# Optimization experiments

Measured on AMD Instinct MI355X. Metric: run time of the kernel, lower is better.

## Reference

```python
import jax, jax.numpy as jnp
import numpy as np

B, LQ, LK, D = 8, 2048, 2048, 512
NEG = -1e9  # stands in for -inf; avoids nan in grads, same softmax result


def setup_inputs() -> dict:
    key = jax.random.key(0)
    kq, kk, kv, km, kr = jax.random.split(key, 5)
    q = jax.random.normal(kq, (B, LQ, D), dtype=jnp.float32)
    k = jax.random.normal(kk, (B, LK, D), dtype=jnp.float32)
    v = jax.random.normal(kv, (B, LK, D), dtype=jnp.float32)
    attn_mask = jax.random.bernoulli(km, 0.1, (B, LK))
    # per-batch positive ratio so masked scores stay very negative after scaling
    ratio = jax.random.uniform(kr, (B,), dtype=jnp.float32, minval=0.5, maxval=1.5)
    scale = jnp.float32(1.0 / np.sqrt(D))
    return {"q": q, "k": k, "v": v, "ratio": ratio, "scale": scale, "attn_mask": attn_mask}


def reference(q, k, v, ratio, scale, attn_mask):
    # QK^T, scale, mask-fill, ratio modulation, softmax, AV
    # (dropout is identity in eval/deterministic baseline)
    scores = jnp.einsum("bqd,bkd->bqk", q, k) * scale          # [B, LQ, LK]
    scores = jnp.where(attn_mask[:, None, :], jnp.float32(NEG), scores)
    scores = scores * ratio[:, None, None]                       # per-batch modulation
    attn = jax.nn.softmax(scores, axis=-1)
    return jnp.einsum("bqk,bkd->bqd", attn, v)                   # [B, LQ, D]
```

## Files before the change

### kernel.cpp

```cpp
#include <hip/hip_runtime.h>
#include <stdint.h>

#define Bn  8
#define LQn 2048
#define LKn 2048
#define Dn  512
#define NT  8

using f32x4  = __attribute__((ext_vector_type(4)))  float;
using f32x16 = __attribute__((ext_vector_type(16))) float;
using bf16x8 = __attribute__((ext_vector_type(8)))  __bf16;
using u16x8  = __attribute__((ext_vector_type(8)))  unsigned short;

#define WS_MASK_OFF 256
#define WS_KP_OFF   (WS_MASK_OFF + Bn*LKn*4)
#define KP_BYTES    ((size_t)Bn*64*32*1024)
#define WS_VP_OFF   (WS_KP_OFF + KP_BYTES)
#define VP_BYTES    ((size_t)Bn*128*16*1024)
#define WS_REQ      ((size_t)WS_VP_OFF + VP_BYTES)

union BFU { __bf16 h; unsigned short u; };
static __device__ __forceinline__ unsigned short f2bfu(float x) { BFU t; t.h = (__bf16)x; return t.u; }

__global__ void mask_prep_kernel(const void* __restrict__ mraw, float* __restrict__ maskadd) {
  __shared__ int sBig, sOff;
  const int tid = threadIdx.x;
  if (tid == 0) { sBig = 0; sOff = 0; }
  __syncthreads();
  const unsigned char* mb = (const unsigned char*)mraw;
  int big = 0, off = 0;
  for (int i = tid; i < Bn*LKn; i += blockDim.x) {
    unsigned char v = mb[i];
    big |= (v > 1) ? 1 : 0;
    off |= (((i & 3) != 0) && v != 0) ? 1 : 0;
  }
  if (big) atomicOr(&sBig, 1);
  if (off) atomicOr(&sOff, 1);
  __syncthreads();
  const int f = sBig ? 2 : (sOff ? 1 : 0);
  for (int i = tid; i < Bn*LKn; i += blockDim.x) {
    bool m;
    if (f == 2)      m = ((const float*)mraw)[i] != 0.0f;
    else if (f == 1) m = mb[i] != 0;
    else             m = ((const int*)mraw)[i] != 0;
    maskadd[i] = m ? -1e30f : 0.0f;
  }
}

__global__ void conv_kp_kernel(const float* __restrict__ k, unsigned short* __restrict__ kp) {
  const int gid = blockIdx.x * 256 + threadIdx.x;
  const int frag = gid >> 6, lane = gid & 63;
  const int b = frag >> 11;
  const int rem = frag & 2047;
  const int kg = rem >> 5, ks = rem & 31;
  const int key = kg*32 + (lane & 31);
  const int hi = lane >> 5;
  const float* src = k + ((size_t)(b*LKn) + key)*Dn + ks*16 + hi*8;
  const f32x4 a = *(const f32x4*)src;
  const f32x4 c = *(const f32x4*)(src + 4);
  u16x8 o;
#pragma unroll
  for (int j = 0; j < 4; ++j) { o[j] = f2bfu(a[j]); o[j+4] = f2bfu(c[j]); }
  *(u16x8*)(kp + (size_t)frag*512 + lane*8) = o;
}

__global__ void conv_vp_kernel(const float* __restrict__ v, unsigned short* __restrict__ vp) {
  __shared__ float vt[16*512];
  const int b = blockIdx.y, kslice = blockIdx.x;
  const float* src = v + ((size_t)(b*LKn) + kslice*16)*Dn;
#pragma unroll
  for (int p = 0; p < 8; ++p) {
    const int idx = p*256 + threadIdx.x;
    *(f32x4*)&vt[idx*4] = *(const f32x4*)(src + (size_t)idx*4);
  }
  __syncthreads();
  unsigned short* dst = vp + ((size_t)(b*128 + kslice)*16)*512;
#pragma unroll
  for (int p = 0; p < 4; ++p) {
    const int slot = p*256 + threadIdx.x;
    const int dg = slot >> 6, lane = slot & 63;
    const int d = dg*32 + (lane & 31);
    const int k0 = (lane >> 5)*8;
    u16x8 o;
#pragma unroll
    for (int j = 0; j < 8; ++j) o[j] = f2bfu(vt[(k0+j)*512 + d]);
    *(u16x8*)(dst + (size_t)dg*512 + lane*8) = o;
  }
}

#define BARRIER_LGKM                                        \
  asm volatile("s_waitcnt lgkmcnt(0)" ::: "memory");        \
  __builtin_amdgcn_s_barrier();                             \
  asm volatile("" ::: "memory");

#define PBUF 32768
#define PQG  16384

__launch_bounds__(512, 2)
__global__ void attn_kernel(const float* __restrict__ q, const unsigned short* __restrict__ kp,
                            const unsigned short* __restrict__ vp,
                            const float* __restrict__ ratio, const float* __restrict__ scalep,
                            const float* __restrict__ maskadd, float* __restrict__ out) {
  __shared__ __align__(16) unsigned short Ql[2*32*512];
  __shared__ __align__(16) unsigned short Pl[2][2*16*512];
  __shared__ __align__(16) float maskl[LKn];
  __shared__ float redl[8][64];

  const int tid = threadIdx.x;
  const int w = tid >> 6, lane = tid & 63;
  const int qc = lane & 31, hi = lane >> 5;
  const int b = blockIdx.x & 7, qtile = blockIdx.x >> 3;
  const int qbase = qtile * 64;
  const float c2 = scalep[0] * ratio[b] * 1.4426950408889634f;

  {
    f32x4 mv = *(const f32x4*)(maskadd + (size_t)b*LKn + tid*4);
#pragma unroll
    for (int j = 0; j < 4; ++j) mv[j] -= 8.0f;
    *(f32x4*)&maskl[tid*4] = mv;
  }

#pragma unroll
  for (int cc = 0; cc < 8; ++cc) {
    const int idx = cc*512 + tid;
    const int hi2 = idx & 1, qc2 = (idx >> 1) & 31, ks2 = (idx >> 6) & 31, qg2 = idx >> 11;
    const float* src = q + ((size_t)(b*LQn) + qbase + qg2*32 + qc2)*Dn + ks2*16 + hi2*8;
    const f32x4 a = *(const f32x4*)src;
    const f32x4 bb = *(const f32x4*)(src + 4);
    u16x8 o;
#pragma unroll
    for (int j = 0; j < 4; ++j) { o[j] = f2bfu(a[j]); o[j+4] = f2bfu(bb[j]); }
    *(u16x8*)((char*)Ql + qg2*32768 + ks2*1024 + hi2*512 + qc2*16) = o;
  }
  __syncthreads();

  f32x16 o00, o01, o10, o11;
#pragma unroll
  for (int r = 0; r < 16; ++r) { o00[r]=0.f; o01[r]=0.f; o10[r]=0.f; o11[r]=0.f; }
  float lacc0 = 0.f, lacc1 = 0.f;

  const char* kpB = (const char*)kp + (size_t)b*2048*1024;
  const char* vpB = (const char*)vp + (size_t)b*2048*1024;
  const int loff = lane*16;
  const char* Qlb = (const char*)Ql + hi*512 + qc*16;
  const char* prc = (const char*)Pl + hi*512 + qc*16;

  bf16x8 pb[32];
  {
    const char* kf0 = kpB + (size_t)w*32768 + loff;
#pragma unroll
    for (int i = 0; i < 32; ++i) pb[i] = *(const bf16x8*)(kf0 + i*1024);
  }

  for (int t = 0; t < NT; ++t) {
    const char* kfn = kpB + (size_t)((t+1 < NT ? t+1 : 0)*8 + w)*32768 + loff;
    const char* vf  = vpB + ((size_t)(t*16)*16 + w*2)*1024 + loff;
    const int tn = (t + 1 < NT) ? 1 : 0;

    f32x4 m4[4];
#pragma unroll
    for (int g = 0; g < 4; ++g)
      m4[g] = *(const f32x4*)&maskl[t*256 + w*32 + g*8 + hi*4];

    f32x16 S0, S1;
#pragma unroll
    for (int r = 0; r < 16; ++r) { S0[r] = 0.f; S1[r] = 0.f; }
    __builtin_amdgcn_s_setprio(1);
#pragma unroll
    for (int i = 0; i < 32; ++i) {
      const bf16x8 kk = pb[i];
      const bf16x8 q0 = *(const bf16x8*)(Qlb + i*1024);
      const bf16x8 q1 = *(const bf16x8*)(Qlb + 32768 + i*1024);
      S0 = __builtin_amdgcn_mfma_f32_32x32x16_bf16(kk, q0, S0, 0, 0, 0);
      S1 = __builtin_amdgcn_mfma_f32_32x32x16_bf16(kk, q1, S1, 0, 0, 0);
      pb[i] = *(const bf16x8*)(vf + (size_t)(i >> 1)*16384 + (i & 1)*1024);
    }
    __builtin_amdgcn_s_setprio(0);

    float ps0 = 0.f, ps1 = 0.f;
    {
      char* pwr = (char*)Pl + (t & 1)*PBUF + (w*2)*1024 + qc*16 + hi*8;
#pragma unroll
      for (int g = 0; g < 4; ++g) {
        const int off = (g >> 1)*1024 + (g & 1)*512;
        float p0 = exp2f(S0[g*4+0]*c2 + m4[g][0]);
        float p1 = exp2f(S0[g*4+1]*c2 + m4[g][1]);
        float p2 = exp2f(S0[g*4+2]*c2 + m4[g][2]);
        float p3 = exp2f(S0[g*4+3]*c2 + m4[g][3]);
        ps0 += (p0 + p1) + (p2 + p3);
        unsigned long long u0 = (unsigned long long)((unsigned int)f2bfu(p0) | ((unsigned int)f2bfu(p1) << 16))
                              | ((unsigned long long)((unsigned int)f2bfu(p2) | ((unsigned int)f2bfu(p3) << 16)) << 32);
        *(unsigned long long*)(pwr + off) = u0;
        p0 = exp2f(S1[g*4+0]*c2 + m4[g][0]);
        p1 = exp2f(S1[g*4+1]*c2 + m4[g][1]);
        p2 = exp2f(S1[g*4+2]*c2 + m4[g][2]);
        p3 = exp2f(S1[g*4+3]*c2 + m4[g][3]);
        ps1 += (p0 + p1) + (p2 + p3);
        unsigned long long u1 = (unsigned long long)((unsigned int)f2bfu(p0) | ((unsigned int)f2bfu(p1) << 16))
                              | ((unsigned long long)((unsigned int)f2bfu(p2) | ((unsigned int)f2bfu(p3) << 16)) << 32);
        *(unsigned long long*)(pwr + PQG + off) = u1;
      }
    }
    ps0 += __shfl_xor(ps0, 32);
    ps1 += __shfl_xor(ps1, 32);
    lacc0 += ps0;
    lacc1 += ps1;

    BARRIER_LGKM;

    const char* prd = prc + (t & 1)*PBUF;
    __builtin_amdgcn_s_setprio(1);
#pragma unroll
    for (int ks2 = 0; ks2 < 16; ++ks2) {
      const int j0 = 2*ks2, j1 = 2*ks2 + 1;
      const bf16x8 pf0 = *(const bf16x8*)(prd + ks2*1024);
      const bf16x8 pf1 = *(const bf16x8*)(prd + PQG + ks2*1024);
      const bf16x8 v0 = pb[j0];
      const bf16x8 v1 = pb[j1];
      o00 = __builtin_amdgcn_mfma_f32_32x32x16_bf16(v0, pf0, o00, 0, 0, 0);
      o10 = __builtin_amdgcn_mfma_f32_32x32x16_bf16(v0, pf1, o10, 0, 0, 0);
      o01 = __builtin_amdgcn_mfma_f32_32x32x16_bf16(v1, pf0, o01, 0, 0, 0);
      o11 = __builtin_amdgcn_mfma_f32_32x32x16_bf16(v1, pf1, o11, 0, 0, 0);
      if (tn) {
        pb[j0] = *(const bf16x8*)(kfn + j0*1024);
        pb[j1] = *(const bf16x8*)(kfn + j1*1024);
      }
    }
    __builtin_amdgcn_s_setprio(0);
  }

  if (lane < 32) { redl[w][qc] = lacc0; redl[w][32 + qc] = lacc1; }
  BARRIER_LGKM;
  float l0 = redl[0][qc], l1 = redl[0][32 + qc];
#pragma unroll
  for (int w2 = 1; w2 < 8; ++w2) { l0 += redl[w2][qc]; l1 += redl[w2][32 + qc]; }

  const float li0 = 1.0f / l0, li1 = 1.0f / l1;
  float* ob0 = out + ((size_t)(b*LQn) + qbase + qc)*Dn + w*64;
  float* ob1 = ob0 + (size_t)32*Dn;
#pragma unroll
  for (int dg = 0; dg < 2; ++dg) {
#pragma unroll
    for (int rq = 0; rq < 4; ++rq) {
      f32x4 ov0, ov1;
#pragma unroll
      for (int c = 0; c < 4; ++c) {
        if (dg == 0) { ov0[c] = o00[rq*4 + c]*li0; ov1[c] = o10[rq*4 + c]*li1; }
        else         { ov0[c] = o01[rq*4 + c]*li0; ov1[c] = o11[rq*4 + c]*li1; }
      }
      *(f32x4*)(ob0 + dg*32 + rq*8 + hi*4) = ov0;
      *(f32x4*)(ob1 + dg*32 + rq*8 + hi*4) = ov1;
    }
  }
}

extern "C" void kernel_launch(void* const* d_in, const int* in_sizes, int n_in,
                              void* d_out, int out_size, void* d_ws, size_t ws_size,
                              hipStream_t stream) {
  const float* q      = (const float*)d_in[0];
  const float* k      = (const float*)d_in[1];
  const float* v      = (const float*)d_in[2];
  const float* ratio  = (const float*)d_in[3];
  const float* scalep = (const float*)d_in[4];
  const void*  mask   = d_in[5];
  float* out = (float*)d_out;
  char* ws = (char*)d_ws;

  if (ws_size < WS_REQ) return;

  float* maskadd      = (float*)(ws + WS_MASK_OFF);
  unsigned short* kpk = (unsigned short*)(ws + WS_KP_OFF);
  unsigned short* vpk = (unsigned short*)(ws + WS_VP_OFF);

  hipLaunchKernelGGL(mask_prep_kernel, dim3(1), dim3(1024), 0, stream, mask, maskadd);
  hipLaunchKernelGGL(conv_kp_kernel, dim3(Bn*64*32*64/256), dim3(256), 0, stream, k, kpk);
  hipLaunchKernelGGL(conv_vp_kernel, dim3(128, Bn), dim3(256), 0, stream, v, vpk);
  hipLaunchKernelGGL(attn_kernel, dim3(Bn*(LQn/64)), dim3(512), 0, stream,
                     q, kpk, vpk, ratio, scalep, maskadd, out);
}
```

Before: 122.3 us.

## Use four waves per block, each covering 128 output columns, with smaller key tiles

Cuts the attention block from 8 to 4 waves. Each wave now accumulates 128 output columns (eight 32x32 accumulators) and processes 16 key tiles of 128 keys instead of 8 tiles of 256. This halves the redundant QK^T recomputation across waves and the P buffer size, but raises per-wave register pressure and the number of barriers. Launch bounds change to 256 threads with 1 block minimum, and the setprio hints are removed.

```diff
diff --git a/kernel.cpp b/kernel.cpp
--- a/kernel.cpp
+++ b/kernel.cpp
@@ -5,7 +5,7 @@
 #define LQn 2048
 #define LKn 2048
 #define Dn  512
-#define NT  8
+#define NT  16
 
 using f32x4  = __attribute__((ext_vector_type(4)))  float;
 using f32x16 = __attribute__((ext_vector_type(16))) float;
@@ -93,18 +93,18 @@
   __builtin_amdgcn_s_barrier();                             \
   asm volatile("" ::: "memory");
 
-#define PBUF 32768
-#define PQG  16384
-
-__launch_bounds__(512, 2)
+#define PBUF 16384
+#define PQG  8192
+
+__launch_bounds__(256, 1)
 __global__ void attn_kernel(const float* __restrict__ q, const unsigned short* __restrict__ kp,
                             const unsigned short* __restrict__ vp,
                             const float* __restrict__ ratio, const float* __restrict__ scalep,
                             const float* __restrict__ maskadd, float* __restrict__ out) {
   __shared__ __align__(16) unsigned short Ql[2*32*512];
-  __shared__ __align__(16) unsigned short Pl[2][2*16*512];
+  __shared__ __align__(16) unsigned short Pl[2][16*512];
   __shared__ __align__(16) float maskl[LKn];
-  __shared__ float redl[8][64];
+  __shared__ float redl[4][64];
 
   const int tid = threadIdx.x;
   const int w = tid >> 6, lane = tid & 63;
@@ -113,16 +113,17 @@
   const int qbase = qtile * 64;
   const float c2 = scalep[0] * ratio[b] * 1.4426950408889634f;
 
-  {
-    f32x4 mv = *(const f32x4*)(maskadd + (size_t)b*LKn + tid*4);
+#pragma unroll
+  for (int p = 0; p < 2; ++p) {
+    f32x4 mv = *(const f32x4*)(maskadd + (size_t)b*LKn + tid*8 + p*4);
 #pragma unroll
     for (int j = 0; j < 4; ++j) mv[j] -= 8.0f;
-    *(f32x4*)&maskl[tid*4] = mv;
-  }
-
-#pragma unroll
-  for (int cc = 0; cc < 8; ++cc) {
-    const int idx = cc*512 + tid;
+    *(f32x4*)&maskl[tid*8 + p*4] = mv;
+  }
+
+#pragma unroll
+  for (int cc = 0; cc < 16; ++cc) {
+    const int idx = cc*256 + tid;
     const int hi2 = idx & 1, qc2 = (idx >> 1) & 31, ks2 = (idx >> 6) & 31, qg2 = idx >> 11;
     const float* src = q + ((size_t)(b*LQn) + qbase + qg2*32 + qc2)*Dn + ks2*16 + hi2*8;
     const f32x4 a = *(const f32x4*)src;
@@ -134,9 +135,12 @@
   }
   __syncthreads();
 
-  f32x16 o00, o01, o10, o11;
-#pragma unroll
-  for (int r = 0; r < 16; ++r) { o00[r]=0.f; o01[r]=0.f; o10[r]=0.f; o11[r]=0.f; }
+  f32x16 o0[4], o1[4];
+#pragma unroll
+  for (int i = 0; i < 4; ++i) {
+#pragma unroll
+    for (int r = 0; r < 16; ++r) { o0[i][r] = 0.f; o1[i][r] = 0.f; }
+  }
   float lacc0 = 0.f, lacc1 = 0.f;
 
   const char* kpB = (const char*)kp + (size_t)b*2048*1024;
@@ -153,19 +157,12 @@
   }
 
   for (int t = 0; t < NT; ++t) {
-    const char* kfn = kpB + (size_t)((t+1 < NT ? t+1 : 0)*8 + w)*32768 + loff;
-    const char* vf  = vpB + ((size_t)(t*16)*16 + w*2)*1024 + loff;
-    const int tn = (t + 1 < NT) ? 1 : 0;
-
-    f32x4 m4[4];
-#pragma unroll
-    for (int g = 0; g < 4; ++g)
-      m4[g] = *(const f32x4*)&maskl[t*256 + w*32 + g*8 + hi*4];
+    const char* vf  = vpB + ((size_t)(t*8)*16 + w*4)*1024 + loff;
+    const char* kfn = kpB + (size_t)(((t+1) & (NT-1))*4 + w)*32768 + loff;
 
     f32x16 S0, S1;
 #pragma unroll
     for (int r = 0; r < 16; ++r) { S0[r] = 0.f; S1[r] = 0.f; }
-    __builtin_amdgcn_s_setprio(1);
 #pragma unroll
     for (int i = 0; i < 32; ++i) {
       const bf16x8 kk = pb[i];
@@ -173,12 +170,15 @@
       const bf16x8 q1 = *(const bf16x8*)(Qlb + 32768 + i*1024);
       S0 = __builtin_amdgcn_mfma_f32_32x32x16_bf16(kk, q0, S0, 0, 0, 0);
       S1 = __builtin_amdgcn_mfma_f32_32x32x16_bf16(kk, q1, S1, 0, 0, 0);
-      pb[i] = *(const bf16x8*)(vf + (size_t)(i >> 1)*16384 + (i & 1)*1024);
-    }
-    __builtin_amdgcn_s_setprio(0);
+      pb[i] = *(const bf16x8*)(vf + (size_t)((i >> 2)*16 + (i & 3))*1024);
+    }
 
     float ps0 = 0.f, ps1 = 0.f;
     {
+      f32x4 m4[4];
+#pragma unroll
+      for (int g = 0; g < 4; ++g)
+        m4[g] = *(const f32x4*)&maskl[t*128 + w*32 + g*8 + hi*4];
       char* pwr = (char*)Pl + (t & 1)*PBUF + (w*2)*1024 + qc*16 + hi*8;
 #pragma unroll
       for (int g = 0; g < 4; ++g) {
@@ -209,47 +209,42 @@
     BARRIER_LGKM;
 
     const char* prd = prc + (t & 1)*PBUF;
-    __builtin_amdgcn_s_setprio(1);
-#pragma unroll
-    for (int ks2 = 0; ks2 < 16; ++ks2) {
-      const int j0 = 2*ks2, j1 = 2*ks2 + 1;
-      const bf16x8 pf0 = *(const bf16x8*)(prd + ks2*1024);
-      const bf16x8 pf1 = *(const bf16x8*)(prd + PQG + ks2*1024);
-      const bf16x8 v0 = pb[j0];
-      const bf16x8 v1 = pb[j1];
-      o00 = __builtin_amdgcn_mfma_f32_32x32x16_bf16(v0, pf0, o00, 0, 0, 0);
-      o10 = __builtin_amdgcn_mfma_f32_32x32x16_bf16(v0, pf1, o10, 0, 0, 0);
-      o01 = __builtin_amdgcn_mfma_f32_32x32x16_bf16(v1, pf0, o01, 0, 0, 0);
-      o11 = __builtin_amdgcn_mfma_f32_32x32x16_bf16(v1, pf1, o11, 0, 0, 0);
-      if (tn) {
-        pb[j0] = *(const bf16x8*)(kfn + j0*1024);
-        pb[j1] = *(const bf16x8*)(kfn + j1*1024);
+#pragma unroll
+    for (int kf = 0; kf < 8; ++kf) {
+      const bf16x8 pf0 = *(const bf16x8*)(prd + kf*1024);
+      const bf16x8 pf1 = *(const bf16x8*)(prd + PQG + kf*1024);
+#pragma unroll
+      for (int dgl = 0; dgl < 4; ++dgl) {
+        const int j = kf*4 + dgl;
+        const bf16x8 vv = pb[j];
+        o0[dgl] = __builtin_amdgcn_mfma_f32_32x32x16_bf16(vv, pf0, o0[dgl], 0, 0, 0);
+        o1[dgl] = __builtin_amdgcn_mfma_f32_32x32x16_bf16(vv, pf1, o1[dgl], 0, 0, 0);
+        pb[j] = *(const bf16x8*)(kfn + j*1024);
       }
     }
-    __builtin_amdgcn_s_setprio(0);
   }
 
   if (lane < 32) { redl[w][qc] = lacc0; redl[w][32 + qc] = lacc1; }
   BARRIER_LGKM;
   float l0 = redl[0][qc], l1 = redl[0][32 + qc];
 #pragma unroll
-  for (int w2 = 1; w2 < 8; ++w2) { l0 += redl[w2][qc]; l1 += redl[w2][32 + qc]; }
+  for (int w2 = 1; w2 < 4; ++w2) { l0 += redl[w2][qc]; l1 += redl[w2][32 + qc]; }
 
   const float li0 = 1.0f / l0, li1 = 1.0f / l1;
-  float* ob0 = out + ((size_t)(b*LQn) + qbase + qc)*Dn + w*64;
+  float* ob0 = out + ((size_t)(b*LQn) + qbase + qc)*Dn + w*128;
   float* ob1 = ob0 + (size_t)32*Dn;
 #pragma unroll
-  for (int dg = 0; dg < 2; ++dg) {
+  for (int dgl = 0; dgl < 4; ++dgl) {
 #pragma unroll
     for (int rq = 0; rq < 4; ++rq) {
       f32x4 ov0, ov1;
 #pragma unroll
       for (int c = 0; c < 4; ++c) {
-        if (dg == 0) { ov0[c] = o00[rq*4 + c]*li0; ov1[c] = o10[rq*4 + c]*li1; }
-        else         { ov0[c] = o01[rq*4 + c]*li0; ov1[c] = o11[rq*4 + c]*li1; }
+        ov0[c] = o0[dgl][rq*4 + c] * li0;
+        ov1[c] = o1[dgl][rq*4 + c] * li1;
       }
-      *(f32x4*)(ob0 + dg*32 + rq*8 + hi*4) = ov0;
-      *(f32x4*)(ob1 + dg*32 + rq*8 + hi*4) = ov1;
+      *(f32x4*)(ob0 + dgl*32 + rq*8 + hi*4) = ov0;
+      *(f32x4*)(ob1 + dgl*32 + rq*8 + hi*4) = ov1;
     }
   }
 }
@@ -275,6 +270,6 @@
   hipLaunchKernelGGL(mask_prep_kernel, dim3(1), dim3(1024), 0, stream, mask, maskadd);
   hipLaunchKernelGGL(conv_kp_kernel, dim3(Bn*64*32*64/256), dim3(256), 0, stream, k, kpk);
   hipLaunchKernelGGL(conv_vp_kernel, dim3(128, Bn), dim3(256), 0, stream, v, vpk);
-  hipLaunchKernelGGL(attn_kernel, dim3(Bn*(LQn/64)), dim3(512), 0, stream,
+  hipLaunchKernelGGL(attn_kernel, dim3(Bn*(LQn/64)), dim3(256), 0, stream,
                      q, kpk, vpk, ratio, scalep, maskadd, out);
 }
```

Result: slower. 159.6 us (+30.6%).
